# Kernel tuning notes

Measured on AMD Instinct MI355X. Metric: run time of the kernel, lower is better.

## Reference

```python
import jax, jax.numpy as jnp
import numpy as np

N, OUT, IN = 16384, 2048, 2048

def setup_inputs() -> dict:
    key = jax.random.key(0)
    k1, k2, k3 = jax.random.split(key, 3)
    input_ = jax.random.normal(k1, (N, IN), dtype=jnp.float32)
    # kaiming normal, fan_in mode: std = sqrt(2/fan_in)
    weight = jax.random.normal(k2, (OUT, IN), dtype=jnp.float32) * np.sqrt(2.0 / IN)
    mask = jax.random.randint(k3, (OUT, IN), 0, 2, dtype=jnp.int32)
    return {"input_": input_, "weight": weight, "mask": mask}

def reference(input_, weight, mask):
    # out = x @ (W * mask)^T  -- mask is a fixed binary expander pattern
    masked_w = weight * mask.astype(weight.dtype)  # [OUT, IN]
    return jnp.matmul(input_, masked_w.T)          # [N, OUT]
```

## Files before the change

### kernel.cpp

```cpp
#include <hip/hip_runtime.h>


#define MDIM 16384
#define NDIM 2048
#define KDIM 2048

#define BM 256
#define BN 256
#define GRID_X ((MDIM / BM) * (NDIM / BN))

using f32x4   = __attribute__((ext_vector_type(4))) float;
using bf16x8  = __attribute__((ext_vector_type(8))) __bf16;
using ushort8 = __attribute__((ext_vector_type(8))) unsigned short;

typedef __attribute__((address_space(3))) const unsigned short* lds_cptr_t;

__device__ __forceinline__ unsigned short f2bf(float f) {
  unsigned int u = __builtin_bit_cast(unsigned int, f);
  u = u + 0x7FFFu + ((u >> 16) & 1u);
  return (unsigned short)(u >> 16);
}


__global__ void convert_input_kernel(const float* __restrict__ in,
                                     unsigned short* __restrict__ out) {
  size_t base = ((size_t)blockIdx.x * blockDim.x + threadIdx.x) * 8;
  float4 a = *reinterpret_cast<const float4*>(in + base);
  float4 b = *reinterpret_cast<const float4*>(in + base + 4);
  ushort8 v;
  v[0] = f2bf(a.x); v[1] = f2bf(a.y); v[2] = f2bf(a.z); v[3] = f2bf(a.w);
  v[4] = f2bf(b.x); v[5] = f2bf(b.y); v[6] = f2bf(b.z); v[7] = f2bf(b.w);
  *reinterpret_cast<ushort8*>(out + base) = v;
}

__global__ void convert_weight_kernel(const float* __restrict__ w,
                                      const int* __restrict__ mk,
                                      unsigned short* __restrict__ out) {
  size_t base = ((size_t)blockIdx.x * blockDim.x + threadIdx.x) * 8;
  float4 a = *reinterpret_cast<const float4*>(w + base);
  float4 b = *reinterpret_cast<const float4*>(w + base + 4);
  int4 m0 = *reinterpret_cast<const int4*>(mk + base);
  int4 m1 = *reinterpret_cast<const int4*>(mk + base + 4);
  ushort8 v;
  v[0] = m0.x ? f2bf(a.x) : (unsigned short)0;
  v[1] = m0.y ? f2bf(a.y) : (unsigned short)0;
  v[2] = m0.z ? f2bf(a.z) : (unsigned short)0;
  v[3] = m0.w ? f2bf(a.w) : (unsigned short)0;
  v[4] = m1.x ? f2bf(b.x) : (unsigned short)0;
  v[5] = m1.y ? f2bf(b.y) : (unsigned short)0;
  v[6] = m1.z ? f2bf(b.z) : (unsigned short)0;
  v[7] = m1.w ? f2bf(b.w) : (unsigned short)0;
  *reinterpret_cast<ushort8*>(out + base) = v;
}


__device__ __forceinline__ f32x4 MF(bf16x8 a, bf16x8 b, f32x4 c) {
  return __builtin_amdgcn_mfma_f32_16x16x32_bf16(a, b, c, 0, 0, 0);
}
#define VMCNT(n) asm volatile("s_waitcnt vmcnt(" #n ")" ::: "memory")
#define LGKM(n)  asm volatile("s_waitcnt lgkmcnt(" #n ")" ::: "memory")
#define DSR(dst, p, off)                                                        \
  asm volatile("ds_read_b128 %0, %1 offset:%2" : "=v"(dst) : "v"(p), "i"(off))

__global__ __launch_bounds__(512, 2) void gemm_1b(
    const unsigned short* __restrict__ Abf,
    const unsigned short* __restrict__ Bbf,
    float* __restrict__ C) {
  __shared__ __attribute__((aligned(16))) unsigned short Asl[4 * 8192];
  __shared__ __attribute__((aligned(16))) unsigned short Bsl[4 * 8192];

  int bid = blockIdx.x;
  int wgs = (bid & 7) * (GRID_X / 8) + (bid >> 3);
  int tm = wgs >> 3;
  int tn = wgs & 7;
  int row0 = tm * BM, col0 = tn * BN;

  int t = threadIdx.x;
  int lane = t & 63, wid = t >> 6;
  int wr = wid >> 2, wc = wid & 3;
  int fr = lane & 15, fq = lane >> 4;

  int p0 = (wid * 2) * 64 + lane;
  int r0 = p0 >> 2, kc0 = ((p0 & 3) ^ ((r0 >> 1) & 3)) * 8;
  size_t offA0 = (size_t)(row0 + r0) * KDIM + kc0;
  size_t offB0 = (size_t)(col0 + r0) * KDIM + kc0;
  int ldsw0 = (wid * 2) * 512;

  int kxor = (fq ^ ((fr >> 1) & 3)) * 8;
  int aoff = (wr * 128 + fr) * 32 + kxor;
  int boff = (wc * 64 + fr) * 32 + kxor;
  lds_cptr_t aA = ((lds_cptr_t)Asl) + aoff;
  lds_cptr_t aB = ((lds_cptr_t)Bsl) + boff;

  f32x4 acc[8][4];
#pragma unroll
  for (int m = 0; m < 8; ++m)
#pragma unroll
    for (int n = 0; n < 4; ++n) acc[m][n] = f32x4{0.f, 0.f, 0.f, 0.f};

  bf16x8 aP[8], bP[4], aQ[8], bQ[4];

#define SLOT_A(b, kh) (Asl + ((b) * 2 + (kh)) * 8192)
#define SLOT_B(b, kh) (Bsl + ((b) * 2 + (kh)) * 8192)

#define STG(slot, base, o0, ke) do {                                            \
  __builtin_amdgcn_global_load_lds(                                             \
      (const __attribute__((address_space(1))) void*)((base) + (o0) + (ke)),    \
      (__attribute__((address_space(3))) void*)((slot) + ldsw0), 16, 0, 0);     \
  __builtin_amdgcn_global_load_lds(                                             \
      (const __attribute__((address_space(1))) void*)((base) + (o0) + 32768 +   \
                                                      (ke)),                    \
      (__attribute__((address_space(3))) void*)((slot) + ldsw0 + 512), 16, 0,   \
      0);                                                                       \
} while (0)

#define RD12(b, kh, AD, BD) do {                                                \
  DSR(AD[0], aA, ((b) * 2 + (kh)) * 16384 + 0 * 1024);                          \
  DSR(AD[1], aA, ((b) * 2 + (kh)) * 16384 + 1 * 1024);                          \
  DSR(AD[2], aA, ((b) * 2 + (kh)) * 16384 + 2 * 1024);                          \
  DSR(AD[3], aA, ((b) * 2 + (kh)) * 16384 + 3 * 1024);                          \
  DSR(AD[4], aA, ((b) * 2 + (kh)) * 16384 + 4 * 1024);                          \
  DSR(AD[5], aA, ((b) * 2 + (kh)) * 16384 + 5 * 1024);                          \
  DSR(AD[6], aA, ((b) * 2 + (kh)) * 16384 + 6 * 1024);                          \
  DSR(AD[7], aA, ((b) * 2 + (kh)) * 16384 + 7 * 1024);                          \
  DSR(BD[0], aB, ((b) * 2 + (kh)) * 16384 + 0 * 1024);                          \
  DSR(BD[1], aB, ((b) * 2 + (kh)) * 16384 + 1 * 1024);                          \
  DSR(BD[2], aB, ((b) * 2 + (kh)) * 16384 + 2 * 1024);                          \
  DSR(BD[3], aB, ((b) * 2 + (kh)) * 16384 + 3 * 1024);                          \
} while (0)

#define PHASE(rb, rkh, AC, BC, AD, BD, STAGES, WAITS) do {                      \
  STAGES;                                                                       \
  WAITS;                                                                        \
  LGKM(0);                                                                      \
  __builtin_amdgcn_s_barrier();                                                 \
  __builtin_amdgcn_sched_barrier(0);                                            \
  __builtin_amdgcn_s_setprio(1);                                                \
  _Pragma("unroll")                                                             \
  for (int _m = 0; _m < 4; ++_m)                                                \
    _Pragma("unroll")                                                           \
    for (int _n = 0; _n < 4; ++_n)                                              \
      acc[_m][_n] = MF(AC[_m], BC[_n], acc[_m][_n]);                            \
  RD12(rb, rkh, AD, BD);                                                        \
  _Pragma("unroll")                                                             \
  for (int _m = 4; _m < 8; ++_m)                                                \
    _Pragma("unroll")                                                           \
    for (int _n = 0; _n < 4; ++_n)                                              \
      acc[_m][_n] = MF(AC[_m], BC[_n], acc[_m][_n]);                            \
  __builtin_amdgcn_s_setprio(0);                                                \
} while (0)

  STG(SLOT_A(0, 0), Abf, offA0, 0);
  STG(SLOT_B(0, 0), Bbf, offB0, 0);
  STG(SLOT_A(0, 1), Abf, offA0, 32);
  STG(SLOT_B(0, 1), Bbf, offB0, 32);
  STG(SLOT_A(1, 0), Abf, offA0, 64);
  STG(SLOT_B(1, 0), Bbf, offB0, 64);
  VMCNT(8);
  __builtin_amdgcn_s_barrier();
  RD12(0, 0, aP, bP);

  for (int i = 0; i < 15; ++i) {
    int kb = i * 128;
    PHASE(0, 1, aP, bP, aQ, bQ, { STG(SLOT_A(1, 1), Abf, offA0, kb + 96);
                                  STG(SLOT_B(1, 1), Bbf, offB0, kb + 96); },
          VMCNT(8));
    PHASE(1, 0, aQ, bQ, aP, bP, { STG(SLOT_A(0, 0), Abf, offA0, kb + 128);
                                  STG(SLOT_B(0, 0), Bbf, offB0, kb + 128); },
          VMCNT(8));
    PHASE(1, 1, aP, bP, aQ, bQ, { STG(SLOT_A(0, 1), Abf, offA0, kb + 160);
                                  STG(SLOT_B(0, 1), Bbf, offB0, kb + 160); },
          VMCNT(8));
    PHASE(0, 0, aQ, bQ, aP, bP, { STG(SLOT_A(1, 0), Abf, offA0, kb + 192);
                                  STG(SLOT_B(1, 0), Bbf, offB0, kb + 192); },
          VMCNT(8));
  }
  PHASE(0, 1, aP, bP, aQ, bQ, { STG(SLOT_A(1, 1), Abf, offA0, 2016);
                                STG(SLOT_B(1, 1), Bbf, offB0, 2016); },
        VMCNT(8));
  PHASE(1, 0, aQ, bQ, aP, bP, , VMCNT(4));
  PHASE(1, 1, aP, bP, aQ, bQ, , VMCNT(0));
  {
    LGKM(0);
    __builtin_amdgcn_sched_barrier(0);
#pragma unroll
    for (int m = 0; m < 8; ++m)
#pragma unroll
      for (int n = 0; n < 4; ++n)
        acc[m][n] = MF(aQ[m], bQ[n], acc[m][n]);
  }

  size_t crow = (size_t)(row0 + wr * 128 + fq * 4);
  int ccol = col0 + wc * 64 + fr;
#pragma unroll
  for (int m = 0; m < 8; ++m)
#pragma unroll
    for (int n = 0; n < 4; ++n) {
      float* cp = C + (crow + m * 16) * NDIM + ccol + n * 16;
#pragma unroll
      for (int e = 0; e < 4; ++e) cp[(size_t)e * NDIM] = acc[m][n][e];
    }
#undef PHASE
#undef RD12
#undef STG
#undef SLOT_A
#undef SLOT_B
}


__global__ __launch_bounds__(256) void gemm_fused_fallback(
    const float* __restrict__ Afp,
    const float* __restrict__ Wfp,
    const int* __restrict__ Mk,
    float* __restrict__ C) {
  __shared__ unsigned short As[128 * 32];
  __shared__ unsigned short Bs[128 * 32];
  int bid = blockIdx.x;
  int nwg = (MDIM / 128) * (NDIM / 128);
  int wg = (bid & 7) * (nwg / 8) + (bid >> 3);
  int tm = wg >> 4, tn = wg & 15;
  int row0 = tm * 128, col0 = tn * 128;
  int t = threadIdx.x;
  int lane = t & 63, wv = t >> 6;
  int wr = wv >> 1, wc = wv & 1;
  int fr = lane & 15, fq = lane >> 4;
  f32x4 acc[4][4];
#pragma unroll
  for (int i = 0; i < 4; ++i)
#pragma unroll
    for (int j = 0; j < 4; ++j) acc[i][j] = f32x4{0.f, 0.f, 0.f, 0.f};
  for (int kt = 0; kt < KDIM; kt += 32) {
#pragma unroll
    for (int j = 0; j < 2; ++j) {
      int c = j * 256 + t;
      int r = c >> 2;
      int ko = (c & 3) * 8;
      const float* ga = Afp + (size_t)(row0 + r) * KDIM + kt + ko;
      float4 a0 = *reinterpret_cast<const float4*>(ga);
      float4 a1 = *reinterpret_cast<const float4*>(ga + 4);
      ushort8 va;
      va[0] = f2bf(a0.x); va[1] = f2bf(a0.y); va[2] = f2bf(a0.z); va[3] = f2bf(a0.w);
      va[4] = f2bf(a1.x); va[5] = f2bf(a1.y); va[6] = f2bf(a1.z); va[7] = f2bf(a1.w);
      *reinterpret_cast<ushort8*>(As + (size_t)c * 8) = va;
      const float* gw = Wfp + (size_t)(col0 + r) * KDIM + kt + ko;
      const int* gm = Mk + (size_t)(col0 + r) * KDIM + kt + ko;
      float4 w0 = *reinterpret_cast<const float4*>(gw);
      float4 w1 = *reinterpret_cast<const float4*>(gw + 4);
      int4 m0 = *reinterpret_cast<const int4*>(gm);
      int4 m1 = *reinterpret_cast<const int4*>(gm + 4);
      ushort8 vb;
      vb[0] = m0.x ? f2bf(w0.x) : (unsigned short)0;
      vb[1] = m0.y ? f2bf(w0.y) : (unsigned short)0;
      vb[2] = m0.z ? f2bf(w0.z) : (unsigned short)0;
      vb[3] = m0.w ? f2bf(w0.w) : (unsigned short)0;
      vb[4] = m1.x ? f2bf(w1.x) : (unsigned short)0;
      vb[5] = m1.y ? f2bf(w1.y) : (unsigned short)0;
      vb[6] = m1.z ? f2bf(w1.z) : (unsigned short)0;
      vb[7] = m1.w ? f2bf(w1.w) : (unsigned short)0;
      *reinterpret_cast<ushort8*>(Bs + (size_t)c * 8) = vb;
    }
    __syncthreads();
    bf16x8 af[4], bfr[4];
#pragma unroll
    for (int m2 = 0; m2 < 4; ++m2)
      af[m2] = *reinterpret_cast<const bf16x8*>(As + (wr * 64 + m2 * 16 + fr) * 32 + fq * 8);
#pragma unroll
    for (int n2 = 0; n2 < 4; ++n2)
      bfr[n2] = *reinterpret_cast<const bf16x8*>(Bs + (wc * 64 + n2 * 16 + fr) * 32 + fq * 8);
#pragma unroll
    for (int m2 = 0; m2 < 4; ++m2)
#pragma unroll
      for (int n2 = 0; n2 < 4; ++n2)
        acc[m2][n2] = MF(af[m2], bfr[n2], acc[m2][n2]);
    __syncthreads();
  }
#pragma unroll
  for (int m2 = 0; m2 < 4; ++m2)
#pragma unroll
    for (int n2 = 0; n2 < 4; ++n2) {
      size_t r0 = (size_t)(row0 + wr * 64 + m2 * 16 + fq * 4);
      size_t c0 = (size_t)(col0 + wc * 64 + n2 * 16 + fr);
#pragma unroll
      for (int i = 0; i < 4; ++i) C[(r0 + i) * NDIM + c0] = acc[m2][n2][i];
    }
}


extern "C" void kernel_launch(void* const* d_in, const int* in_sizes, int n_in,
                              void* d_out, int out_size, void* d_ws, size_t ws_size,
                              hipStream_t stream) {
  const float* input  = (const float*)d_in[0];
  const float* weight = (const float*)d_in[1];
  const int*   mask   = (const int*)d_in[2];
  float* out = (float*)d_out;

  const size_t needA = (size_t)MDIM * KDIM * sizeof(unsigned short);
  const size_t needB = (size_t)NDIM * KDIM * sizeof(unsigned short);

  if (ws_size >= needA + needB) {
    unsigned short* Abf = (unsigned short*)d_ws;
    unsigned short* Bbf = (unsigned short*)((char*)d_ws + needA);
    convert_input_kernel<<<(MDIM * (size_t)KDIM / 8) / 256, 256, 0, stream>>>(input, Abf);
    convert_weight_kernel<<<(NDIM * (size_t)KDIM / 8) / 256, 256, 0, stream>>>(weight, mask, Bbf);
    gemm_1b<<<GRID_X, 512, 0, stream>>>(Abf, Bbf, out);
  } else {
    int nwg = (MDIM / 128) * (NDIM / 128);
    gemm_fused_fallback<<<nwg, 256, 0, stream>>>(input, weight, mask, out);
  }
}
```

Baseline: 167.5 us.

## Shrink GEMM tile to 256x128 with 4 waves for higher occupancy

Replaces the 512-thread 256x256 tile kernel with a 256-thread 256x128 tile kernel that targets three workgroups per CU, halving the LDS footprint. The four-slot k-pipeline with partial vmcnt waits becomes a simple double buffer of 32-wide k slices that issues loads right after a full vmcnt(0) barrier. The aim is to hide latency through occupancy rather than deep software pipelining. In exchange, each CU loads more B per FLOP, and the full wait each phase exposes more load latency inside each workgroup.

```diff
diff --git a/kernel.cpp b/kernel.cpp
--- a/kernel.cpp
+++ b/kernel.cpp
@@ -6,7 +6,7 @@
 #define KDIM 2048
 
 #define BM 256
-#define BN 256
+#define BN 128
 #define GRID_X ((MDIM / BM) * (NDIM / BN))
 
 using f32x4   = __attribute__((ext_vector_type(4))) float;
@@ -62,29 +62,29 @@
 #define DSR(dst, p, off)                                                        \
   asm volatile("ds_read_b128 %0, %1 offset:%2" : "=v"(dst) : "v"(p), "i"(off))
 
-__global__ __launch_bounds__(512, 2) void gemm_1b(
+__global__ __launch_bounds__(256, 3) void gemm_occ(
     const unsigned short* __restrict__ Abf,
     const unsigned short* __restrict__ Bbf,
     float* __restrict__ C) {
-  __shared__ __attribute__((aligned(16))) unsigned short Asl[4 * 8192];
-  __shared__ __attribute__((aligned(16))) unsigned short Bsl[4 * 8192];
+  __shared__ __attribute__((aligned(16))) unsigned short Asl[2 * 8192];
+  __shared__ __attribute__((aligned(16))) unsigned short Bsl[2 * 4096];
 
   int bid = blockIdx.x;
   int wgs = (bid & 7) * (GRID_X / 8) + (bid >> 3);
-  int tm = wgs >> 3;
-  int tn = wgs & 7;
+  int tm = wgs >> 4;
+  int tn = wgs & 15;
   int row0 = tm * BM, col0 = tn * BN;
 
   int t = threadIdx.x;
   int lane = t & 63, wid = t >> 6;
-  int wr = wid >> 2, wc = wid & 3;
+  int wr = wid >> 1, wc = wid & 1;
   int fr = lane & 15, fq = lane >> 4;
 
-  int p0 = (wid * 2) * 64 + lane;
+  int p0 = wid * 64 + lane;
   int r0 = p0 >> 2, kc0 = ((p0 & 3) ^ ((r0 >> 1) & 3)) * 8;
   size_t offA0 = (size_t)(row0 + r0) * KDIM + kc0;
   size_t offB0 = (size_t)(col0 + r0) * KDIM + kc0;
-  int ldsw0 = (wid * 2) * 512;
+  int ldsw = wid * 512;
 
   int kxor = (fq ^ ((fr >> 1) & 3)) * 8;
   int aoff = (wr * 128 + fr) * 32 + kxor;
@@ -100,40 +100,48 @@
 
   bf16x8 aP[8], bP[4], aQ[8], bQ[4];
 
-#define SLOT_A(b, kh) (Asl + ((b) * 2 + (kh)) * 8192)
-#define SLOT_B(b, kh) (Bsl + ((b) * 2 + (kh)) * 8192)
-
-#define STG(slot, base, o0, ke) do {                                            \
-  __builtin_amdgcn_global_load_lds(                                             \
-      (const __attribute__((address_space(1))) void*)((base) + (o0) + (ke)),    \
-      (__attribute__((address_space(3))) void*)((slot) + ldsw0), 16, 0, 0);     \
-  __builtin_amdgcn_global_load_lds(                                             \
-      (const __attribute__((address_space(1))) void*)((base) + (o0) + 32768 +   \
-                                                      (ke)),                    \
-      (__attribute__((address_space(3))) void*)((slot) + ldsw0 + 512), 16, 0,   \
-      0);                                                                       \
-} while (0)
-
-#define RD12(b, kh, AD, BD) do {                                                \
-  DSR(AD[0], aA, ((b) * 2 + (kh)) * 16384 + 0 * 1024);                          \
-  DSR(AD[1], aA, ((b) * 2 + (kh)) * 16384 + 1 * 1024);                          \
-  DSR(AD[2], aA, ((b) * 2 + (kh)) * 16384 + 2 * 1024);                          \
-  DSR(AD[3], aA, ((b) * 2 + (kh)) * 16384 + 3 * 1024);                          \
-  DSR(AD[4], aA, ((b) * 2 + (kh)) * 16384 + 4 * 1024);                          \
-  DSR(AD[5], aA, ((b) * 2 + (kh)) * 16384 + 5 * 1024);                          \
-  DSR(AD[6], aA, ((b) * 2 + (kh)) * 16384 + 6 * 1024);                          \
-  DSR(AD[7], aA, ((b) * 2 + (kh)) * 16384 + 7 * 1024);                          \
-  DSR(BD[0], aB, ((b) * 2 + (kh)) * 16384 + 0 * 1024);                          \
-  DSR(BD[1], aB, ((b) * 2 + (kh)) * 16384 + 1 * 1024);                          \
-  DSR(BD[2], aB, ((b) * 2 + (kh)) * 16384 + 2 * 1024);                          \
-  DSR(BD[3], aB, ((b) * 2 + (kh)) * 16384 + 3 * 1024);                          \
-} while (0)
-
-#define PHASE(rb, rkh, AC, BC, AD, BD, STAGES, WAITS) do {                      \
-  STAGES;                                                                       \
-  WAITS;                                                                        \
+#define STGA(sa, ke) do {                                                       \
+  _Pragma("unroll")                                                             \
+  for (int _j = 0; _j < 4; ++_j)                                                \
+    __builtin_amdgcn_global_load_lds(                                           \
+        (const __attribute__((address_space(1))) void*)(Abf + offA0 +           \
+                                                        _j * 131072 + (ke)),    \
+        (__attribute__((address_space(3))) void*)(Asl + (sa) * 8192 +           \
+                                                  _j * 2048 + ldsw),            \
+        16, 0, 0);                                                              \
+} while (0)
+#define STGB(sb, ke) do {                                                       \
+  _Pragma("unroll")                                                             \
+  for (int _j = 0; _j < 2; ++_j)                                                \
+    __builtin_amdgcn_global_load_lds(                                           \
+        (const __attribute__((address_space(1))) void*)(Bbf + offB0 +           \
+                                                        _j * 131072 + (ke)),    \
+        (__attribute__((address_space(3))) void*)(Bsl + (sb) * 4096 +           \
+                                                  _j * 2048 + ldsw),            \
+        16, 0, 0);                                                              \
+} while (0)
+
+#define RD12(s, AD, BD) do {                                                    \
+  DSR(AD[0], aA, (s) * 16384 + 0 * 1024);                                       \
+  DSR(BD[0], aB, (s) * 8192 + 0 * 1024);                                        \
+  DSR(BD[1], aB, (s) * 8192 + 1 * 1024);                                        \
+  DSR(BD[2], aB, (s) * 8192 + 2 * 1024);                                        \
+  DSR(BD[3], aB, (s) * 8192 + 3 * 1024);                                        \
+  DSR(AD[1], aA, (s) * 16384 + 1 * 1024);                                       \
+  DSR(AD[2], aA, (s) * 16384 + 2 * 1024);                                       \
+  DSR(AD[3], aA, (s) * 16384 + 3 * 1024);                                       \
+  DSR(AD[4], aA, (s) * 16384 + 4 * 1024);                                       \
+  DSR(AD[5], aA, (s) * 16384 + 5 * 1024);                                       \
+  DSR(AD[6], aA, (s) * 16384 + 6 * 1024);                                       \
+  DSR(AD[7], aA, (s) * 16384 + 7 * 1024);                                       \
+} while (0)
+
+#define PHASE(rs, AC, BC, AD, BD, STAGES) do {                                  \
+  VMCNT(0);                                                                     \
   LGKM(0);                                                                      \
   __builtin_amdgcn_s_barrier();                                                 \
+  __builtin_amdgcn_sched_barrier(0);                                            \
+  STAGES;                                                                       \
   __builtin_amdgcn_sched_barrier(0);                                            \
   __builtin_amdgcn_s_setprio(1);                                                \
   _Pragma("unroll")                                                             \
@@ -141,7 +149,7 @@
     _Pragma("unroll")                                                           \
     for (int _n = 0; _n < 4; ++_n)                                              \
       acc[_m][_n] = MF(AC[_m], BC[_n], acc[_m][_n]);                            \
-  RD12(rb, rkh, AD, BD);                                                        \
+  RD12(rs, AD, BD);                                                             \
   _Pragma("unroll")                                                             \
   for (int _m = 4; _m < 8; ++_m)                                                \
     _Pragma("unroll")                                                           \
@@ -150,36 +158,18 @@
   __builtin_amdgcn_s_setprio(0);                                                \
 } while (0)
 
-  STG(SLOT_A(0, 0), Abf, offA0, 0);
-  STG(SLOT_B(0, 0), Bbf, offB0, 0);
-  STG(SLOT_A(0, 1), Abf, offA0, 32);
-  STG(SLOT_B(0, 1), Bbf, offB0, 32);
-  STG(SLOT_A(1, 0), Abf, offA0, 64);
-  STG(SLOT_B(1, 0), Bbf, offB0, 64);
-  VMCNT(8);
+  STGA(0, 0);  STGB(0, 0);
+  STGA(1, 32); STGB(1, 32);
+  VMCNT(6);
   __builtin_amdgcn_s_barrier();
-  RD12(0, 0, aP, bP);
-
-  for (int i = 0; i < 15; ++i) {
-    int kb = i * 128;
-    PHASE(0, 1, aP, bP, aQ, bQ, { STG(SLOT_A(1, 1), Abf, offA0, kb + 96);
-                                  STG(SLOT_B(1, 1), Bbf, offB0, kb + 96); },
-          VMCNT(8));
-    PHASE(1, 0, aQ, bQ, aP, bP, { STG(SLOT_A(0, 0), Abf, offA0, kb + 128);
-                                  STG(SLOT_B(0, 0), Bbf, offB0, kb + 128); },
-          VMCNT(8));
-    PHASE(1, 1, aP, bP, aQ, bQ, { STG(SLOT_A(0, 1), Abf, offA0, kb + 160);
-                                  STG(SLOT_B(0, 1), Bbf, offB0, kb + 160); },
-          VMCNT(8));
-    PHASE(0, 0, aQ, bQ, aP, bP, { STG(SLOT_A(1, 0), Abf, offA0, kb + 192);
-                                  STG(SLOT_B(1, 0), Bbf, offB0, kb + 192); },
-          VMCNT(8));
-  }
-  PHASE(0, 1, aP, bP, aQ, bQ, { STG(SLOT_A(1, 1), Abf, offA0, 2016);
-                                STG(SLOT_B(1, 1), Bbf, offB0, 2016); },
-        VMCNT(8));
-  PHASE(1, 0, aQ, bQ, aP, bP, , VMCNT(4));
-  PHASE(1, 1, aP, bP, aQ, bQ, , VMCNT(0));
+  RD12(0, aP, bP);
+
+  for (int i = 0; i < 31; ++i) {
+    int kb = i * 64;
+    PHASE(1, aP, bP, aQ, bQ, { STGA(0, kb + 64); STGB(0, kb + 64); });
+    PHASE(0, aQ, bQ, aP, bP, { STGA(1, kb + 96); STGB(1, kb + 96); });
+  }
+  PHASE(1, aP, bP, aQ, bQ, );
   {
     LGKM(0);
     __builtin_amdgcn_sched_barrier(0);
@@ -202,9 +192,8 @@
     }
 #undef PHASE
 #undef RD12
-#undef STG
-#undef SLOT_A
-#undef SLOT_B
+#undef STGA
+#undef STGB
 }
 
 
@@ -302,7 +291,7 @@
     unsigned short* Bbf = (unsigned short*)((char*)d_ws + needA);
     convert_input_kernel<<<(MDIM * (size_t)KDIM / 8) / 256, 256, 0, stream>>>(input, Abf);
     convert_weight_kernel<<<(NDIM * (size_t)KDIM / 8) / 256, 256, 0, stream>>>(weight, mask, Bbf);
-    gemm_1b<<<GRID_X, 512, 0, stream>>>(Abf, Bbf, out);
+    gemm_occ<<<GRID_X, 256, 0, stream>>>(Abf, Bbf, out);
   } else {
     int nwg = (MDIM / 128) * (NDIM / 128);
     gemm_fused_fallback<<<nwg, 256, 0, stream>>>(input, weight, mask, out);
```

Result: slower. 592.9 us (+253.9%).
